# Kernel tuning notes

Measured on AMD Instinct MI355X. Metric: run time of the kernel, lower is better.

Reference implementation:

```python
import jax, jax.numpy as jnp
import numpy as np

D = 768
H = 12
HD = D // H
EPS = 1e-8  # torch cosine_similarity default eps


def setup_inputs() -> dict:
    key = jax.random.key(0)
    ks = jax.random.split(key, 16)
    bs, T, K = 8, 2048, 512
    s = 0.02
    return {
        "hidden_states": jax.random.normal(ks[0], (bs, T, D), jnp.float32),
        "attention_mask": jnp.ones((bs, T), jnp.int32),
        "pooled_hidden_states": jax.random.normal(ks[1], (bs, D), jnp.float32),
        "kg_key": jax.random.normal(ks[2], (bs, K, D), jnp.float32),
        "kg_value": jax.random.normal(ks[3], (bs, K, D), jnp.float32),
        "beta": jnp.ones((H,), jnp.float32),
        "Wq": jax.random.normal(ks[4], (D, D), jnp.float32) * s,
        "bq": jnp.zeros((D,), jnp.float32),
        "Wk": jax.random.normal(ks[5], (D, D), jnp.float32) * s,
        "bk": jnp.zeros((D,), jnp.float32),
        "Wv": jax.random.normal(ks[6], (D, D), jnp.float32) * s,
        "bv": jnp.zeros((D,), jnp.float32),
        "Wo": jax.random.normal(ks[7], (D, D), jnp.float32) * s,
        "bo": jnp.zeros((D,), jnp.float32),
    }


def reference(hidden_states, attention_mask, pooled_hidden_states, kg_key, kg_value,
              beta, Wq, bq, Wk, bk, Wv, bv, Wo, bo):
    bs, T, _ = hidden_states.shape
    K = kg_key.shape[1]
    # cosine similarity between pooled state and each KG key: [bs, K]
    pn = pooled_hidden_states / jnp.maximum(
        jnp.linalg.norm(pooled_hidden_states, axis=-1, keepdims=True), EPS)
    kn = kg_key / jnp.maximum(jnp.linalg.norm(kg_key, axis=-1, keepdims=True), EPS)
    sim = jnp.einsum("bd,bkd->bk", pn, kn)

    scale = HD ** -0.5
    # projections (torch Linear: y = x @ W.T + b)
    q = ((hidden_states @ Wq.T + bq) * scale).reshape(bs, T, H, HD).transpose(0, 2, 1, 3)
    k = (kg_value @ Wk.T + bk).reshape(bs, K, H, HD).transpose(0, 2, 1, 3)
    v = (kg_value @ Wv.T + bv).reshape(bs, K, H, HD).transpose(0, 2, 1, 3)

    # scores + per-head cosine-sim bias: [bs, H, T, K]
    scores = jnp.einsum("bhtd,bhkd->bhtk", q, k)
    scores = scores + beta[None, :, None, None] * sim[:, None, None, :]
    probs = jax.nn.softmax(scores, axis=-1)

    out = jnp.einsum("bhtk,bhkd->bhtd", probs, v)
    out = out.transpose(0, 2, 1, 3).reshape(bs, T, D)
    return out @ Wo.T + bo
```

## Files before the change

kernel.cpp:

```cpp
#include <hip/hip_runtime.h>
#include <math.h>

#define D_MODEL 768
#define NHEAD   12
#define HD      64
#define SEQ_T   2048
#define SEQ_K   512
#define BS      8
#define EPS_COS 1e-8f
#define LOG2E   1.44269504f

typedef short  bf16x8 __attribute__((ext_vector_type(8)));
typedef float  f32x4  __attribute__((ext_vector_type(4)));

__device__ __forceinline__ ushort f2bf(float x) {
    unsigned b = __float_as_uint(x);
    return (ushort)((b + 0x7FFF + ((b >> 16) & 1)) >> 16);
}
__device__ __forceinline__ unsigned cvt_pk_bf16(float lo, float hi) {
    unsigned r;
    asm("v_cvt_pk_bf16_f32 %0, %1, %2" : "=v"(r) : "v"(lo), "v"(hi));
    return r;
}
__device__ __forceinline__ float exp2_fast(float x) {
    float r;
    asm("v_exp_f32 %0, %1" : "=v"(r) : "v"(x));
    return r;
}

__device__ __forceinline__ void async_copy16(void* lds_base, const void* g_src) {
    __builtin_amdgcn_global_load_lds(
        (const __attribute__((address_space(1))) unsigned int*)g_src,
        (__attribute__((address_space(3))) unsigned int*)lds_base,
        16, 0, 0);
}

__global__ __launch_bounds__(256) void cvt4_kernel(
    const float* __restrict__ s0, const float* __restrict__ s1,
    const float* __restrict__ s2, const float* __restrict__ s3,
    ushort* __restrict__ d0, ushort* __restrict__ d1,
    ushort* __restrict__ d2, ushort* __restrict__ d3)
{
    const float* s; ushort* d;
    switch (blockIdx.y) {
        case 0: s = s0; d = d0; break;
        case 1: s = s1; d = d1; break;
        case 2: s = s2; d = d2; break;
        default: s = s3; d = d3; break;
    }
    int i = blockIdx.x * 256 + threadIdx.x;
    float4 v = reinterpret_cast<const float4*>(s)[i];
    ushort4 o;
    o.x = f2bf(v.x); o.y = f2bf(v.y); o.z = f2bf(v.z); o.w = f2bf(v.w);
    reinterpret_cast<ushort4*>(d)[i] = o;
}

__global__ __launch_bounds__(256) void sim_kernel(
    const float* __restrict__ pooled, const float* __restrict__ kg_key,
    const float* __restrict__ beta, float* __restrict__ bsim)
{
    int wid  = (blockIdx.x * blockDim.x + threadIdx.x) >> 6;
    int lane = threadIdx.x & 63;
    int b  = wid >> 9;
    int kk = wid & 511;
    const float* p   = pooled + (size_t)b * D_MODEL;
    const float* key = kg_key + ((size_t)b * SEQ_K + kk) * D_MODEL;
    float dpk = 0.f, dkk = 0.f, dpp = 0.f;
    for (int i = lane; i < D_MODEL; i += 64) {
        float pv = p[i], kv = key[i];
        dpk += pv * kv; dkk += kv * kv; dpp += pv * pv;
    }
    for (int off = 32; off; off >>= 1) {
        dpk += __shfl_xor(dpk, off);
        dkk += __shfl_xor(dkk, off);
        dpp += __shfl_xor(dpp, off);
    }
    if (lane == 0) {
        float np_ = fmaxf(sqrtf(dpp), EPS_COS);
        float nk_ = fmaxf(sqrtf(dkk), EPS_COS);
        float sv = (dpk / (np_ * nk_)) * LOG2E;
#pragma unroll
        for (int h = 0; h < NHEAD; ++h)
            bsim[(size_t)(b * NHEAD + h) * SEQ_K + kk] = beta[h] * sv;
    }
}

__global__ __launch_bounds__(256, 3) void gemm_q_a32_kernel(
    const float* __restrict__ A, const ushort* __restrict__ W,
    const float* __restrict__ bias, ushort* __restrict__ out_bf, float scale)
{
    constexpr int Kd = D_MODEL;
    __shared__ __align__(16) float  AsF[128 * 64];
    __shared__ __align__(16) ushort Bs[128 * 64];
    const int tid = threadIdx.x, wid = tid >> 6, l = tid & 63;
    const int g = l >> 4, c = l & 15;
    const int m0 = blockIdx.x * 128, n0 = blockIdx.y * 128;
    const int wm = (wid >> 1) * 64, wn = (wid & 1) * 64;

    f32x4 acc[4][4] = {};

    for (int k0 = 0; k0 < Kd; k0 += 64) {
        __syncthreads();
#pragma unroll
        for (int it = 0; it < 8; ++it) {
            int L = wid * 8192 + it * 1024 + l * 16;
            int row = L >> 8;
            int blk = (L >> 4) & 15;
            int gb = (blk & 8) | ((blk & 7) ^ (row & 7));
            async_copy16((char*)AsF + wid * 8192 + it * 1024,
                         A + (size_t)(m0 + row) * Kd + k0 + gb * 4);
        }
#pragma unroll
        for (int it = 0; it < 4; ++it) {
            int L = wid * 4096 + it * 1024 + l * 16;
            int row = L >> 7;
            int gb = ((L >> 4) & 7) ^ (row & 7);
            async_copy16((char*)Bs + wid * 4096 + it * 1024,
                         W + (size_t)(n0 + row) * Kd + k0 + gb * 8);
        }
        __syncthreads();

        bf16x8 af[4][2], bf[4][2];
#pragma unroll
        for (int mt = 0; mt < 4; ++mt)
#pragma unroll
            for (int ks = 0; ks < 2; ++ks) {
                int row = wm + mt * 16 + c;
                int b0 = ks * 8 + 2 * g;
                int p0 = (b0 & 8) | ((b0 & 7) ^ (row & 7));
                int p1 = (b0 & 8) | (((b0 + 1) & 7) ^ (row & 7));
                f32x4 a0 = *(const f32x4*)((const char*)AsF + row * 256 + (p0 << 4));
                f32x4 a1 = *(const f32x4*)((const char*)AsF + row * 256 + (p1 << 4));
                union { unsigned u[4]; bf16x8 v; } t;
                t.u[0] = cvt_pk_bf16(a0[0], a0[1]);
                t.u[1] = cvt_pk_bf16(a0[2], a0[3]);
                t.u[2] = cvt_pk_bf16(a1[0], a1[1]);
                t.u[3] = cvt_pk_bf16(a1[2], a1[3]);
                af[mt][ks] = t.v;
            }
#pragma unroll
        for (int nt = 0; nt < 4; ++nt)
#pragma unroll
            for (int ks = 0; ks < 2; ++ks) {
                int row = wn + nt * 16 + c;
                bf[nt][ks] = *(const bf16x8*)((const char*)Bs + row * 128 +
                                              (((ks * 4 + g) ^ (row & 7)) << 4));
            }
        __builtin_amdgcn_s_setprio(1);
#pragma unroll
        for (int mt = 0; mt < 4; ++mt)
#pragma unroll
            for (int nt = 0; nt < 4; ++nt) {
                acc[mt][nt] = __builtin_amdgcn_mfma_f32_16x16x32_bf16(
                    af[mt][0], bf[nt][0], acc[mt][nt], 0, 0, 0);
                acc[mt][nt] = __builtin_amdgcn_mfma_f32_16x16x32_bf16(
                    af[mt][1], bf[nt][1], acc[mt][nt], 0, 0, 0);
            }
        __builtin_amdgcn_s_setprio(0);
    }

#pragma unroll
    for (int mt = 0; mt < 4; ++mt)
#pragma unroll
        for (int nt = 0; nt < 4; ++nt) {
            int col = n0 + wn + nt * 16 + c;
            float bv = bias[col];
#pragma unroll
            for (int j = 0; j < 4; ++j) {
                int row = m0 + wm + mt * 16 + g * 4 + j;
                out_bf[(size_t)row * Kd + col] = f2bf((acc[mt][nt][j] + bv) * scale);
            }
        }
}

__global__ __launch_bounds__(256, 3) void gemm_kv_a32_kernel(
    const float* __restrict__ A,
    const ushort* __restrict__ Wk_, const float* __restrict__ bk_,
    const ushort* __restrict__ Wv_, const float* __restrict__ bv_,
    ushort* __restrict__ outk, ushort* __restrict__ vt)
{
    constexpr int Kd = D_MODEL;
    __shared__ __align__(16) float  AsF[64 * 64];
    __shared__ __align__(16) ushort Bk[64 * 64];
    __shared__ __align__(16) ushort Bv[64 * 64];
    const int tid = threadIdx.x, wid = tid >> 6, l = tid & 63;
    const int g = l >> 4, c = l & 15;
    const int m0 = blockIdx.x * 64, h = blockIdx.y, n0 = h * 64;
    const int wm = (wid >> 1) * 32, wn = (wid & 1) * 32;

    f32x4 acck[2][2] = {}, accv[2][2] = {};

    for (int k0 = 0; k0 < Kd; k0 += 64) {
        __syncthreads();
#pragma unroll
        for (int it = 0; it < 4; ++it) {
            int L = wid * 4096 + it * 1024 + l * 16;
            int row = L >> 8;
            int blk = (L >> 4) & 15;
            int gb = (blk & 8) | ((blk & 7) ^ (row & 7));
            async_copy16((char*)AsF + wid * 4096 + it * 1024,
                         A + (size_t)(m0 + row) * Kd + k0 + gb * 4);
        }
#pragma unroll
        for (int it = 0; it < 2; ++it) {
            int L = wid * 2048 + it * 1024 + l * 16;
            int row = L >> 7;
            int gb = ((L >> 4) & 7) ^ (row & 7);
            async_copy16((char*)Bk + wid * 2048 + it * 1024,
                         Wk_ + (size_t)(n0 + row) * Kd + k0 + gb * 8);
            async_copy16((char*)Bv + wid * 2048 + it * 1024,
                         Wv_ + (size_t)(n0 + row) * Kd + k0 + gb * 8);
        }
        __syncthreads();

        bf16x8 af[2][2], bkf[2][2], bvf[2][2];
#pragma unroll
        for (int mt = 0; mt < 2; ++mt)
#pragma unroll
            for (int ks = 0; ks < 2; ++ks) {
                int row = wm + mt * 16 + c;
                int b0 = ks * 8 + 2 * g;
                int p0 = (b0 & 8) | ((b0 & 7) ^ (row & 7));
                int p1 = (b0 & 8) | (((b0 + 1) & 7) ^ (row & 7));
                f32x4 a0 = *(const f32x4*)((const char*)AsF + row * 256 + (p0 << 4));
                f32x4 a1 = *(const f32x4*)((const char*)AsF + row * 256 + (p1 << 4));
                union { unsigned u[4]; bf16x8 v; } t;
                t.u[0] = cvt_pk_bf16(a0[0], a0[1]);
                t.u[1] = cvt_pk_bf16(a0[2], a0[3]);
                t.u[2] = cvt_pk_bf16(a1[0], a1[1]);
                t.u[3] = cvt_pk_bf16(a1[2], a1[3]);
                af[mt][ks] = t.v;
            }
#pragma unroll
        for (int nt = 0; nt < 2; ++nt)
#pragma unroll
            for (int ks = 0; ks < 2; ++ks) {
                int row = wn + nt * 16 + c;
                int off = row * 128 + (((ks * 4 + g) ^ (row & 7)) << 4);
                bkf[nt][ks] = *(const bf16x8*)((const char*)Bk + off);
                bvf[nt][ks] = *(const bf16x8*)((const char*)Bv + off);
            }
        __builtin_amdgcn_s_setprio(1);
#pragma unroll
        for (int mt = 0; mt < 2; ++mt)
#pragma unroll
            for (int nt = 0; nt < 2; ++nt)
#pragma unroll
                for (int ks = 0; ks < 2; ++ks) {
                    acck[mt][nt] = __builtin_amdgcn_mfma_f32_16x16x32_bf16(
                        af[mt][ks], bkf[nt][ks], acck[mt][nt], 0, 0, 0);
                    accv[mt][nt] = __builtin_amdgcn_mfma_f32_16x16x32_bf16(
                        af[mt][ks], bvf[nt][ks], accv[mt][nt], 0, 0, 0);
                }
        __builtin_amdgcn_s_setprio(0);
    }

#pragma unroll
    for (int mt = 0; mt < 2; ++mt)
#pragma unroll
        for (int nt = 0; nt < 2; ++nt) {
            int col = n0 + wn + nt * 16 + c;
            float bbk = bk_[col];
#pragma unroll
            for (int j = 0; j < 4; ++j) {
                int row = m0 + wm + mt * 16 + 4 * g + j;
                outk[(size_t)row * Kd + col] = f2bf(acck[mt][nt][j] + bbk);
            }
        }

    {
        int b = m0 >> 9;
        int kc = (m0 >> 7) & 3;
#pragma unroll
        for (int mt = 0; mt < 2; ++mt) {
            int kb0 = (m0 & 64) + wm + mt * 16 + 4 * g;
            int kp0 = ((kb0 >> 5) << 5) | (((kb0 >> 2) & 3) << 3) | (((kb0 >> 4) & 1) << 2);
#pragma unroll
            for (int nt = 0; nt < 2; ++nt) {
                int d = wn + nt * 16 + c;
                float bbv = bv_[n0 + d];
                unsigned u0 = cvt_pk_bf16(accv[mt][nt][0] + bbv, accv[mt][nt][1] + bbv);
                unsigned u1 = cvt_pk_bf16(accv[mt][nt][2] + bbv, accv[mt][nt][3] + bbv);
                size_t base = ((size_t)(b * NHEAD + h) * HD + d) * SEQ_K + kc * 128 + kp0;
                uint2 st2; st2.x = u0; st2.y = u1;
                *(uint2*)(vt + base) = st2;
            }
        }
    }
}

__global__ __launch_bounds__(256, 2) void gemm_o_kernel(
    const ushort* __restrict__ A, const ushort* __restrict__ W,
    const float* __restrict__ bias, float* __restrict__ out_f32)
{
    constexpr int Kd = D_MODEL;
    __shared__ __align__(16) ushort As[128 * 64];
    __shared__ __align__(16) ushort Bs[128 * 64];
    const int tid = threadIdx.x, wid = tid >> 6, l = tid & 63;
    const int g = l >> 4, c = l & 15;
    const int m0 = blockIdx.x * 128, n0 = blockIdx.y * 128;
    const int wm = (wid >> 1) * 64, wn = (wid & 1) * 64;

    f32x4 acc[4][4] = {};

    for (int k0 = 0; k0 < Kd; k0 += 64) {
        __syncthreads();
#pragma unroll
        for (int it = 0; it < 4; ++it) {
            int L = wid * 4096 + it * 1024 + l * 16;
            int row = L >> 7;
            int gb = ((L >> 4) & 7) ^ (row & 7);
            async_copy16((char*)As + wid * 4096 + it * 1024,
                         A + (size_t)(m0 + row) * Kd + k0 + gb * 8);
        }
#pragma unroll
        for (int it = 0; it < 4; ++it) {
            int L = wid * 4096 + it * 1024 + l * 16;
            int row = L >> 7;
            int gb = ((L >> 4) & 7) ^ (row & 7);
            async_copy16((char*)Bs + wid * 4096 + it * 1024,
                         W + (size_t)(n0 + row) * Kd + k0 + gb * 8);
        }
        __syncthreads();

        bf16x8 af[4][2], bf[4][2];
#pragma unroll
        for (int mt = 0; mt < 4; ++mt)
#pragma unroll
            for (int ks = 0; ks < 2; ++ks) {
                int row = wm + mt * 16 + c;
                af[mt][ks] = *(const bf16x8*)((const char*)As + row * 128 +
                                              (((ks * 4 + g) ^ (row & 7)) << 4));
            }
#pragma unroll
        for (int nt = 0; nt < 4; ++nt)
#pragma unroll
            for (int ks = 0; ks < 2; ++ks) {
                int row = wn + nt * 16 + c;
                bf[nt][ks] = *(const bf16x8*)((const char*)Bs + row * 128 +
                                              (((ks * 4 + g) ^ (row & 7)) << 4));
            }
        __builtin_amdgcn_s_setprio(1);
#pragma unroll
        for (int mt = 0; mt < 4; ++mt)
#pragma unroll
            for (int nt = 0; nt < 4; ++nt) {
                acc[mt][nt] = __builtin_amdgcn_mfma_f32_16x16x32_bf16(
                    af[mt][0], bf[nt][0], acc[mt][nt], 0, 0, 0);
                acc[mt][nt] = __builtin_amdgcn_mfma_f32_16x16x32_bf16(
                    af[mt][1], bf[nt][1], acc[mt][nt], 0, 0, 0);
            }
        __builtin_amdgcn_s_setprio(0);
    }

#pragma unroll
    for (int mt = 0; mt < 4; ++mt)
#pragma unroll
        for (int nt = 0; nt < 4; ++nt) {
            int col = n0 + wn + nt * 16 + c;
            float bv = bias[col];
#pragma unroll
            for (int j = 0; j < 4; ++j) {
                int row = m0 + wm + mt * 16 + g * 4 + j;
                out_f32[(size_t)row * Kd + col] = acc[mt][nt][j] + bv;
            }
        }
}

__global__ __launch_bounds__(256, 4) void attn_mfma_kernel(
    const ushort* __restrict__ qb, const ushort* __restrict__ kbp,
    const ushort* __restrict__ vt, const float* __restrict__ bsim,
    ushort* __restrict__ ctx)
{
    int bid = blockIdx.x;
    int w = (bid & 7) * 384 + (bid >> 3);
    int tt = w & 31; int rest = w >> 5; int h = rest % 12; int b = rest / 12;
    int t0 = tt * 64;
    int tid = threadIdx.x, wid = tid >> 6, l = tid & 63;
    int g = l >> 4, c = l & 15;

    __shared__ __align__(16) ushort Ks[128 * 64];
    __shared__ __align__(16) ushort Vs[64 * 128];

    const ushort* srck[4]; const ushort* srcv[4];
    char* dstk[4]; char* dstv[4];
#pragma unroll
    for (int it = 0; it < 4; ++it) {
        int L = wid * 4096 + it * 1024 + l * 16;
        int row = L >> 7;
        int gb = ((L >> 4) & 7) ^ (row & 7);
        srck[it] = kbp + (size_t)(b * SEQ_K + row) * D_MODEL + h * HD + gb * 8;
        dstk[it] = (char*)Ks + wid * 4096 + it * 1024;
        int d = L >> 8;
        int blk = (L >> 4) & 15;
        int gblk = (blk & 8) | ((blk & 7) ^ (d & 7));
        srcv[it] = vt + ((size_t)((b * NHEAD + h) * HD + d)) * SEQ_K + gblk * 8;
        dstv[it] = (char*)Vs + wid * 4096 + it * 1024;
    }

#pragma unroll
    for (int it = 0; it < 2; ++it) {
        int L = wid * 2048 + it * 1024 + l * 16;
        int row = L >> 7;
        int gb = ((L >> 4) & 7) ^ (row & 7);
        async_copy16((char*)Vs + wid * 2048 + it * 1024,
                     qb + (size_t)(b * SEQ_T + t0 + row) * D_MODEL + h * HD + gb * 8);
    }
#pragma unroll
    for (int it = 0; it < 4; ++it) async_copy16(dstk[it], srck[it]);
    const float* bsrow = bsim + (size_t)(b * NHEAD + h) * SEQ_K;
    __syncthreads();

    bf16x8 aq[2];
#pragma unroll
    for (int ks = 0; ks < 2; ++ks) {
        int row = wid * 16 + c;
        aq[ks] = *(const bf16x8*)((const char*)Vs + row * 128 +
                                  (((ks * 4 + g) ^ (row & 7)) << 4));
    }
    __syncthreads();

    const bf16x8 ones8 = {(short)0x3F80, (short)0x3F80, (short)0x3F80, (short)0x3F80,
                          (short)0x3F80, (short)0x3F80, (short)0x3F80, (short)0x3F80};
    f32x4 oacc[4] = {};
    f32x4 oSum = {};

    for (int kc = 0; kc < 4; ++kc) {
#pragma unroll
        for (int it = 0; it < 4; ++it) {
            async_copy16(dstv[it], srcv[it]);
            srcv[it] += 128;
        }
        f32x4 st[8];
        __builtin_amdgcn_s_setprio(1);
#pragma unroll
        for (int nt = 0; nt < 8; ++nt) {
            f32x4 cinit = *(const f32x4*)(bsrow + kc * 128 + nt * 16 + 4 * g);
            int krow = nt * 16 + c;
            bf16x8 ak0 = *(const bf16x8*)((const char*)Ks + krow * 128 +
                                          ((g ^ (krow & 7)) << 4));
            st[nt] = __builtin_amdgcn_mfma_f32_16x16x32_bf16(
                ak0, aq[0], cinit, 0, 0, 0);
            bf16x8 ak1 = *(const bf16x8*)((const char*)Ks + krow * 128 +
                                          (((4 + g) ^ (krow & 7)) << 4));
            st[nt] = __builtin_amdgcn_mfma_f32_16x16x32_bf16(
                ak1, aq[1], st[nt], 0, 0, 0);
        }
        __builtin_amdgcn_s_setprio(0);

#pragma unroll
        for (int nt = 0; nt < 8; ++nt)
#pragma unroll
            for (int j = 0; j < 4; ++j) st[nt][j] = exp2_fast(st[nt][j]);

        __syncthreads();

        if (kc < 3) {
#pragma unroll
            for (int it = 0; it < 4; ++it) {
                srck[it] += 128 * D_MODEL;
                async_copy16(dstk[it], srck[it]);
            }
        }

        bf16x8 pa[4];
#pragma unroll
        for (int kb = 0; kb < 4; ++kb) {
            union { unsigned u[4]; bf16x8 v; } pk;
            pk.u[0] = cvt_pk_bf16(st[2 * kb][0],     st[2 * kb][1]);
            pk.u[1] = cvt_pk_bf16(st[2 * kb][2],     st[2 * kb][3]);
            pk.u[2] = cvt_pk_bf16(st[2 * kb + 1][0], st[2 * kb + 1][1]);
            pk.u[3] = cvt_pk_bf16(st[2 * kb + 1][2], st[2 * kb + 1][3]);
            pa[kb] = pk.v;
        }
        __builtin_amdgcn_s_setprio(1);
#pragma unroll
        for (int kb = 0; kb < 4; ++kb) {
            oSum = __builtin_amdgcn_mfma_f32_16x16x32_bf16(
                pa[kb], ones8, oSum, 0, 0, 0);
#pragma unroll
            for (int dt = 0; dt < 4; ++dt) {
                int d = dt * 16 + c;
                int blk = kb * 4 + g;
                int sb = (blk & 8) | ((blk & 7) ^ (d & 7));
                bf16x8 bv = *(const bf16x8*)((const char*)Vs + d * 256 + sb * 16);
                oacc[dt] = __builtin_amdgcn_mfma_f32_16x16x32_bf16(
                    pa[kb], bv, oacc[dt], 0, 0, 0);
            }
        }
        __builtin_amdgcn_s_setprio(0);
        __syncthreads();
    }

    f32x4 invL;
#pragma unroll
    for (int j = 0; j < 4; ++j) invL[j] = 1.f / oSum[j];
#pragma unroll
    for (int dt = 0; dt < 4; ++dt)
#pragma unroll
        for (int j = 0; j < 4; ++j) {
            int trow = t0 + wid * 16 + 4 * g + j;
            int d = dt * 16 + c;
            ctx[(size_t)(b * SEQ_T + trow) * D_MODEL + h * HD + d] =
                f2bf(oacc[dt][j] * invL[j]);
        }
}

extern "C" void kernel_launch(void* const* d_in, const int* in_sizes, int n_in,
                              void* d_out, int out_size, void* d_ws, size_t ws_size,
                              hipStream_t stream)
{
    const float* hidden  = (const float*)d_in[0];
    const float* pooled  = (const float*)d_in[2];
    const float* kg_key  = (const float*)d_in[3];
    const float* kg_val  = (const float*)d_in[4];
    const float* beta    = (const float*)d_in[5];
    const float* Wq = (const float*)d_in[6];  const float* bq = (const float*)d_in[7];
    const float* Wk = (const float*)d_in[8];  const float* bk = (const float*)d_in[9];
    const float* Wv = (const float*)d_in[10]; const float* bv = (const float*)d_in[11];
    const float* Wo = (const float*)d_in[12]; const float* bo = (const float*)d_in[13];
    float* out = (float*)d_out;

    const size_t MQ = (size_t)BS * SEQ_T;
    const size_t MK = (size_t)BS * SEQ_K;
    const size_t DW = D_MODEL * D_MODEL;

    float*  bsim = (float*)d_ws;
    ushort* wqb  = (ushort*)(bsim + BS * NHEAD * SEQ_K);
    ushort* wkb  = wqb + DW;
    ushort* wvb  = wkb + DW;
    ushort* wob  = wvb + DW;
    ushort* qbb  = wob + DW;
    ushort* kbb  = qbb + MQ * D_MODEL;
    ushort* vtb  = kbb + MK * D_MODEL;
    ushort* ctxb = vtb + MK * D_MODEL;

    cvt4_kernel<<<dim3(DW / 4 / 256, 4), 256, 0, stream>>>(
        Wq, Wk, Wv, Wo, wqb, wkb, wvb, wob);

    sim_kernel<<<(BS * SEQ_K) / 4, 256, 0, stream>>>(pooled, kg_key, beta, bsim);

    gemm_q_a32_kernel<<<dim3(MQ / 128, 6), 256, 0, stream>>>(
        hidden, wqb, bq, qbb, 0.125f * LOG2E);
    gemm_kv_a32_kernel<<<dim3(MK / 64, 12), 256, 0, stream>>>(
        kg_val, wkb, bk, wvb, bv, kbb, vtb);

    attn_mfma_kernel<<<BS * NHEAD * (SEQ_T / 64), 256, 0, stream>>>(
        qbb, kbb, vtb, bsim, ctxb);

    gemm_o_kernel<<<dim3(MQ / 128, 6), 256, 0, stream>>>(ctxb, wob, bo, out);
}
```

Before: 128.3 us.

## Read Q, K, V fragments directly from global memory instead of LDS staging

```diff
diff --git a/kernel.cpp b/kernel.cpp
--- a/kernel.cpp
+++ b/kernel.cpp
@@ -379,70 +379,32 @@
     int tid = threadIdx.x, wid = tid >> 6, l = tid & 63;
     int g = l >> 4, c = l & 15;
 
-    __shared__ __align__(16) ushort Ks[128 * 64];
-    __shared__ __align__(16) ushort Vs[64 * 128];
-
-    const ushort* srck[4]; const ushort* srcv[4];
-    char* dstk[4]; char* dstv[4];
-#pragma unroll
-    for (int it = 0; it < 4; ++it) {
-        int L = wid * 4096 + it * 1024 + l * 16;
-        int row = L >> 7;
-        int gb = ((L >> 4) & 7) ^ (row & 7);
-        srck[it] = kbp + (size_t)(b * SEQ_K + row) * D_MODEL + h * HD + gb * 8;
-        dstk[it] = (char*)Ks + wid * 4096 + it * 1024;
-        int d = L >> 8;
-        int blk = (L >> 4) & 15;
-        int gblk = (blk & 8) | ((blk & 7) ^ (d & 7));
-        srcv[it] = vt + ((size_t)((b * NHEAD + h) * HD + d)) * SEQ_K + gblk * 8;
-        dstv[it] = (char*)Vs + wid * 4096 + it * 1024;
-    }
-
-#pragma unroll
-    for (int it = 0; it < 2; ++it) {
-        int L = wid * 2048 + it * 1024 + l * 16;
-        int row = L >> 7;
-        int gb = ((L >> 4) & 7) ^ (row & 7);
-        async_copy16((char*)Vs + wid * 2048 + it * 1024,
-                     qb + (size_t)(b * SEQ_T + t0 + row) * D_MODEL + h * HD + gb * 8);
-    }
-#pragma unroll
-    for (int it = 0; it < 4; ++it) async_copy16(dstk[it], srck[it]);
-    const float* bsrow = bsim + (size_t)(b * NHEAD + h) * SEQ_K;
-    __syncthreads();
-
+    const float*  bsrow = bsim + (size_t)(b * NHEAD + h) * SEQ_K;
+    const ushort* qrow = qb + (size_t)(b * SEQ_T + t0 + wid * 16 + c) * D_MODEL + h * HD;
     bf16x8 aq[2];
-#pragma unroll
-    for (int ks = 0; ks < 2; ++ks) {
-        int row = wid * 16 + c;
-        aq[ks] = *(const bf16x8*)((const char*)Vs + row * 128 +
-                                  (((ks * 4 + g) ^ (row & 7)) << 4));
-    }
-    __syncthreads();
+    aq[0] = *(const bf16x8*)(qrow + g * 8);
+    aq[1] = *(const bf16x8*)(qrow + (4 + g) * 8);
+
+    const ushort* krow = kbp + (size_t)(b * SEQ_K + c) * D_MODEL + h * HD;
+    const ushort* vrow = vt + ((size_t)((b * NHEAD + h) * HD) + c) * SEQ_K;
 
     const bf16x8 ones8 = {(short)0x3F80, (short)0x3F80, (short)0x3F80, (short)0x3F80,
                           (short)0x3F80, (short)0x3F80, (short)0x3F80, (short)0x3F80};
     f32x4 oacc[4] = {};
     f32x4 oSum = {};
 
+#pragma unroll
     for (int kc = 0; kc < 4; ++kc) {
-#pragma unroll
-        for (int it = 0; it < 4; ++it) {
-            async_copy16(dstv[it], srcv[it]);
-            srcv[it] += 128;
-        }
         f32x4 st[8];
         __builtin_amdgcn_s_setprio(1);
 #pragma unroll
         for (int nt = 0; nt < 8; ++nt) {
             f32x4 cinit = *(const f32x4*)(bsrow + kc * 128 + nt * 16 + 4 * g);
-            int krow = nt * 16 + c;
-            bf16x8 ak0 = *(const bf16x8*)((const char*)Ks + krow * 128 +
-                                          ((g ^ (krow & 7)) << 4));
+            const ushort* kr = krow + (size_t)(kc * 128 + nt * 16) * D_MODEL;
+            bf16x8 ak0 = *(const bf16x8*)(kr + g * 8);
+            bf16x8 ak1 = *(const bf16x8*)(kr + (4 + g) * 8);
             st[nt] = __builtin_amdgcn_mfma_f32_16x16x32_bf16(
                 ak0, aq[0], cinit, 0, 0, 0);
-            bf16x8 ak1 = *(const bf16x8*)((const char*)Ks + krow * 128 +
-                                          (((4 + g) ^ (krow & 7)) << 4));
             st[nt] = __builtin_amdgcn_mfma_f32_16x16x32_bf16(
                 ak1, aq[1], st[nt], 0, 0, 0);
         }
@@ -452,16 +414,6 @@
         for (int nt = 0; nt < 8; ++nt)
 #pragma unroll
             for (int j = 0; j < 4; ++j) st[nt][j] = exp2_fast(st[nt][j]);
-
-        __syncthreads();
-
-        if (kc < 3) {
-#pragma unroll
-            for (int it = 0; it < 4; ++it) {
-                srck[it] += 128 * D_MODEL;
-                async_copy16(dstk[it], srck[it]);
-            }
-        }
 
         bf16x8 pa[4];
 #pragma unroll
@@ -480,16 +432,13 @@
                 pa[kb], ones8, oSum, 0, 0, 0);
 #pragma unroll
             for (int dt = 0; dt < 4; ++dt) {
-                int d = dt * 16 + c;
-                int blk = kb * 4 + g;
-                int sb = (blk & 8) | ((blk & 7) ^ (d & 7));
-                bf16x8 bv = *(const bf16x8*)((const char*)Vs + d * 256 + sb * 16);
+                bf16x8 bv = *(const bf16x8*)(vrow + (size_t)(dt * 16) * SEQ_K +
+                                             kc * 128 + (kb * 4 + g) * 8);
                 oacc[dt] = __builtin_amdgcn_mfma_f32_16x16x32_bf16(
                     pa[kb], bv, oacc[dt], 0, 0, 0);
             }
         }
         __builtin_amdgcn_s_setprio(0);
-        __syncthreads();
     }
 
     f32x4 invL;
```

Result: slower. 268.0 us (+108.9%).

## Process 128 query rows per attention block to reuse K/V tiles

Applied to the files above, without the earlier changes.

```diff
diff --git a/kernel.cpp b/kernel.cpp
--- a/kernel.cpp
+++ b/kernel.cpp
@@ -367,15 +367,15 @@
         }
 }
 
-__global__ __launch_bounds__(256, 4) void attn_mfma_kernel(
+__global__ __launch_bounds__(256, 2) void attn_mfma_kernel(
     const ushort* __restrict__ qb, const ushort* __restrict__ kbp,
     const ushort* __restrict__ vt, const float* __restrict__ bsim,
     ushort* __restrict__ ctx)
 {
     int bid = blockIdx.x;
-    int w = (bid & 7) * 384 + (bid >> 3);
-    int tt = w & 31; int rest = w >> 5; int h = rest % 12; int b = rest / 12;
-    int t0 = tt * 64;
+    int w = (bid & 7) * 192 + (bid >> 3);
+    int tile = w & 15; int rest = w >> 4; int h = rest % 12; int b = rest / 12;
+    int t0 = tile * 128;
     int tid = threadIdx.x, wid = tid >> 6, l = tid & 63;
     int g = l >> 4, c = l & 15;
 
@@ -399,11 +399,11 @@
     }
 
 #pragma unroll
-    for (int it = 0; it < 2; ++it) {
-        int L = wid * 2048 + it * 1024 + l * 16;
+    for (int it = 0; it < 4; ++it) {
+        int L = wid * 4096 + it * 1024 + l * 16;
         int row = L >> 7;
         int gb = ((L >> 4) & 7) ^ (row & 7);
-        async_copy16((char*)Vs + wid * 2048 + it * 1024,
+        async_copy16((char*)Vs + wid * 4096 + it * 1024,
                      qb + (size_t)(b * SEQ_T + t0 + row) * D_MODEL + h * HD + gb * 8);
     }
 #pragma unroll
@@ -411,19 +411,21 @@
     const float* bsrow = bsim + (size_t)(b * NHEAD + h) * SEQ_K;
     __syncthreads();
 
-    bf16x8 aq[2];
-#pragma unroll
-    for (int ks = 0; ks < 2; ++ks) {
-        int row = wid * 16 + c;
-        aq[ks] = *(const bf16x8*)((const char*)Vs + row * 128 +
-                                  (((ks * 4 + g) ^ (row & 7)) << 4));
-    }
+    bf16x8 aq[2][2];
+#pragma unroll
+    for (int sub = 0; sub < 2; ++sub)
+#pragma unroll
+        for (int ks = 0; ks < 2; ++ks) {
+            int row = wid * 32 + sub * 16 + c;
+            aq[sub][ks] = *(const bf16x8*)((const char*)Vs + row * 128 +
+                                           (((ks * 4 + g) ^ (row & 7)) << 4));
+        }
     __syncthreads();
 
     const bf16x8 ones8 = {(short)0x3F80, (short)0x3F80, (short)0x3F80, (short)0x3F80,
                           (short)0x3F80, (short)0x3F80, (short)0x3F80, (short)0x3F80};
-    f32x4 oacc[4] = {};
-    f32x4 oSum = {};
+    f32x4 oacc0[4] = {}, oacc1[4] = {};
+    f32x4 oSum0 = {}, oSum1 = {};
 
     for (int kc = 0; kc < 4; ++kc) {
 #pragma unroll
@@ -431,7 +433,7 @@
             async_copy16(dstv[it], srcv[it]);
             srcv[it] += 128;
         }
-        f32x4 st[8];
+        f32x4 st0[8], st1[8];
         __builtin_amdgcn_s_setprio(1);
 #pragma unroll
         for (int nt = 0; nt < 8; ++nt) {
@@ -439,19 +441,26 @@
             int krow = nt * 16 + c;
             bf16x8 ak0 = *(const bf16x8*)((const char*)Ks + krow * 128 +
                                           ((g ^ (krow & 7)) << 4));
-            st[nt] = __builtin_amdgcn_mfma_f32_16x16x32_bf16(
-                ak0, aq[0], cinit, 0, 0, 0);
+            st0[nt] = __builtin_amdgcn_mfma_f32_16x16x32_bf16(
+                ak0, aq[0][0], cinit, 0, 0, 0);
+            st1[nt] = __builtin_amdgcn_mfma_f32_16x16x32_bf16(
+                ak0, aq[1][0], cinit, 0, 0, 0);
             bf16x8 ak1 = *(const bf16x8*)((const char*)Ks + krow * 128 +
                                           (((4 + g) ^ (krow & 7)) << 4));
-            st[nt] = __builtin_amdgcn_mfma_f32_16x16x32_bf16(
-                ak1, aq[1], st[nt], 0, 0, 0);
+            st0[nt] = __builtin_amdgcn_mfma_f32_16x16x32_bf16(
+                ak1, aq[0][1], st0[nt], 0, 0, 0);
+            st1[nt] = __builtin_amdgcn_mfma_f32_16x16x32_bf16(
+                ak1, aq[1][1], st1[nt], 0, 0, 0);
         }
         __builtin_amdgcn_s_setprio(0);
 
 #pragma unroll
         for (int nt = 0; nt < 8; ++nt)
 #pragma unroll
-            for (int j = 0; j < 4; ++j) st[nt][j] = exp2_fast(st[nt][j]);
+            for (int j = 0; j < 4; ++j) {
+                st0[nt][j] = exp2_fast(st0[nt][j]);
+                st1[nt][j] = exp2_fast(st1[nt][j]);
+            }
 
         __syncthreads();
 
@@ -463,46 +472,61 @@
             }
         }
 
-        bf16x8 pa[4];
+        bf16x8 pa0[4], pa1[4];
 #pragma unroll
         for (int kb = 0; kb < 4; ++kb) {
             union { unsigned u[4]; bf16x8 v; } pk;
-            pk.u[0] = cvt_pk_bf16(st[2 * kb][0],     st[2 * kb][1]);
-            pk.u[1] = cvt_pk_bf16(st[2 * kb][2],     st[2 * kb][3]);
-            pk.u[2] = cvt_pk_bf16(st[2 * kb + 1][0], st[2 * kb + 1][1]);
-            pk.u[3] = cvt_pk_bf16(st[2 * kb + 1][2], st[2 * kb + 1][3]);
-            pa[kb] = pk.v;
+            pk.u[0] = cvt_pk_bf16(st0[2 * kb][0],     st0[2 * kb][1]);
+            pk.u[1] = cvt_pk_bf16(st0[2 * kb][2],     st0[2 * kb][3]);
+            pk.u[2] = cvt_pk_bf16(st0[2 * kb + 1][0], st0[2 * kb + 1][1]);
+            pk.u[3] = cvt_pk_bf16(st0[2 * kb + 1][2], st0[2 * kb + 1][3]);
+            pa0[kb] = pk.v;
+            pk.u[0] = cvt_pk_bf16(st1[2 * kb][0],     st1[2 * kb][1]);
+            pk.u[1] = cvt_pk_bf16(st1[2 * kb][2],     st1[2 * kb][3]);
+            pk.u[2] = cvt_pk_bf16(st1[2 * kb + 1][0], st1[2 * kb + 1][1]);
+            pk.u[3] = cvt_pk_bf16(st1[2 * kb + 1][2], st1[2 * kb + 1][3]);
+            pa1[kb] = pk.v;
         }
         __builtin_amdgcn_s_setprio(1);
 #pragma unroll
         for (int kb = 0; kb < 4; ++kb) {
-            oSum = __builtin_amdgcn_mfma_f32_16x16x32_bf16(
-                pa[kb], ones8, oSum, 0, 0, 0);
+            oSum0 = __builtin_amdgcn_mfma_f32_16x16x32_bf16(
+                pa0[kb], ones8, oSum0, 0, 0, 0);
+            oSum1 = __builtin_amdgcn_mfma_f32_16x16x32_bf16(
+                pa1[kb], ones8, oSum1, 0, 0, 0);
 #pragma unroll
             for (int dt = 0; dt < 4; ++dt) {
                 int d = dt * 16 + c;
                 int blk = kb * 4 + g;
                 int sb = (blk & 8) | ((blk & 7) ^ (d & 7));
                 bf16x8 bv = *(const bf16x8*)((const char*)Vs + d * 256 + sb * 16);
-                oacc[dt] = __builtin_amdgcn_mfma_f32_16x16x32_bf16(
-                    pa[kb], bv, oacc[dt], 0, 0, 0);
+                oacc0[dt] = __builtin_amdgcn_mfma_f32_16x16x32_bf16(
+                    pa0[kb], bv, oacc0[dt], 0, 0, 0);
+                oacc1[dt] = __builtin_amdgcn_mfma_f32_16x16x32_bf16(
+                    pa1[kb], bv, oacc1[dt], 0, 0, 0);
             }
         }
         __builtin_amdgcn_s_setprio(0);
         __syncthreads();
     }
 
-    f32x4 invL;
-#pragma unroll
-    for (int j = 0; j < 4; ++j) invL[j] = 1.f / oSum[j];
+    f32x4 invL0, invL1;
+#pragma unroll
+    for (int j = 0; j < 4; ++j) {
+        invL0[j] = 1.f / oSum0[j];
+        invL1[j] = 1.f / oSum1[j];
+    }
 #pragma unroll
     for (int dt = 0; dt < 4; ++dt)
 #pragma unroll
         for (int j = 0; j < 4; ++j) {
-            int trow = t0 + wid * 16 + 4 * g + j;
             int d = dt * 16 + c;
-            ctx[(size_t)(b * SEQ_T + trow) * D_MODEL + h * HD + d] =
-                f2bf(oacc[dt][j] * invL[j]);
+            int trow0 = t0 + wid * 32 + 4 * g + j;
+            ctx[(size_t)(b * SEQ_T + trow0) * D_MODEL + h * HD + d] =
+                f2bf(oacc0[dt][j] * invL0[j]);
+            int trow1 = trow0 + 16;
+            ctx[(size_t)(b * SEQ_T + trow1) * D_MODEL + h * HD + d] =
+                f2bf(oacc1[dt][j] * invL1[j]);
         }
 }
 
@@ -545,7 +569,7 @@
     gemm_kv_a32_kernel<<<dim3(MK / 64, 12), 256, 0, stream>>>(
         kg_val, wkb, bk, wvb, bv, kbb, vtb);
 
-    attn_mfma_kernel<<<BS * NHEAD * (SEQ_T / 64), 256, 0, stream>>>(
+    attn_mfma_kernel<<<BS * NHEAD * (SEQ_T / 128), 256, 0, stream>>>(
         qbb, kbb, vtb, bsim, ctxb);
 
     gemm_o_kernel<<<dim3(MQ / 128, 6), 256, 0, stream>>>(ctxb, wob, bo, out);
```

After: 122.6 us. 4.4% less time.

## Enlarge attention tile to 256 query rows with double-buffered K/V

Applied to the files above, without the earlier changes.

```diff
diff --git a/kernel.cpp b/kernel.cpp
--- a/kernel.cpp
+++ b/kernel.cpp
@@ -367,143 +367,161 @@
         }
 }
 
-__global__ __launch_bounds__(256, 4) void attn_mfma_kernel(
+__global__ __launch_bounds__(256, 2) void attn_mfma_kernel(
     const ushort* __restrict__ qb, const ushort* __restrict__ kbp,
     const ushort* __restrict__ vt, const float* __restrict__ bsim,
     ushort* __restrict__ ctx)
 {
     int bid = blockIdx.x;
-    int w = (bid & 7) * 384 + (bid >> 3);
-    int tt = w & 31; int rest = w >> 5; int h = rest % 12; int b = rest / 12;
-    int t0 = tt * 64;
+    int w = (bid & 7) * 96 + (bid >> 3);
+    int tile = w & 7; int rest = w >> 3; int h = rest % 12; int b = rest / 12;
+    int t0 = tile * 256;
     int tid = threadIdx.x, wid = tid >> 6, l = tid & 63;
     int g = l >> 4, c = l & 15;
 
-    __shared__ __align__(16) ushort Ks[128 * 64];
-    __shared__ __align__(16) ushort Vs[64 * 128];
+    __shared__ __align__(16) ushort KV[2][128 * 128];
 
     const ushort* srck[4]; const ushort* srcv[4];
-    char* dstk[4]; char* dstv[4];
+    int offk[4], offv[4];
 #pragma unroll
     for (int it = 0; it < 4; ++it) {
         int L = wid * 4096 + it * 1024 + l * 16;
         int row = L >> 7;
         int gb = ((L >> 4) & 7) ^ (row & 7);
         srck[it] = kbp + (size_t)(b * SEQ_K + row) * D_MODEL + h * HD + gb * 8;
-        dstk[it] = (char*)Ks + wid * 4096 + it * 1024;
+        offk[it] = wid * 4096 + it * 1024;
         int d = L >> 8;
         int blk = (L >> 4) & 15;
         int gblk = (blk & 8) | ((blk & 7) ^ (d & 7));
         srcv[it] = vt + ((size_t)((b * NHEAD + h) * HD + d)) * SEQ_K + gblk * 8;
-        dstv[it] = (char*)Vs + wid * 4096 + it * 1024;
-    }
-
-#pragma unroll
-    for (int it = 0; it < 2; ++it) {
-        int L = wid * 2048 + it * 1024 + l * 16;
+        offv[it] = 16384 + wid * 4096 + it * 1024;
+    }
+
+#pragma unroll
+    for (int it = 0; it < 8; ++it) {
+        int L = wid * 8192 + it * 1024 + l * 16;
         int row = L >> 7;
         int gb = ((L >> 4) & 7) ^ (row & 7);
-        async_copy16((char*)Vs + wid * 2048 + it * 1024,
+        async_copy16((char*)KV[0] + wid * 8192 + it * 1024,
                      qb + (size_t)(b * SEQ_T + t0 + row) * D_MODEL + h * HD + gb * 8);
     }
-#pragma unroll
-    for (int it = 0; it < 4; ++it) async_copy16(dstk[it], srck[it]);
     const float* bsrow = bsim + (size_t)(b * NHEAD + h) * SEQ_K;
     __syncthreads();
 
-    bf16x8 aq[2];
-#pragma unroll
-    for (int ks = 0; ks < 2; ++ks) {
-        int row = wid * 16 + c;
-        aq[ks] = *(const bf16x8*)((const char*)Vs + row * 128 +
-                                  (((ks * 4 + g) ^ (row & 7)) << 4));
-    }
+    bf16x8 aq[4][2];
+#pragma unroll
+    for (int sub = 0; sub < 4; ++sub)
+#pragma unroll
+        for (int ks = 0; ks < 2; ++ks) {
+            int row = wid * 64 + sub * 16 + c;
+            aq[sub][ks] = *(const bf16x8*)((const char*)KV[0] + row * 128 +
+                                           (((ks * 4 + g) ^ (row & 7)) << 4));
+        }
     __syncthreads();
+
+#pragma unroll
+    for (int it = 0; it < 4; ++it) {
+        async_copy16((char*)KV[0] + offk[it], srck[it]);
+        async_copy16((char*)KV[0] + offv[it], srcv[it]);
+    }
 
     const bf16x8 ones8 = {(short)0x3F80, (short)0x3F80, (short)0x3F80, (short)0x3F80,
                           (short)0x3F80, (short)0x3F80, (short)0x3F80, (short)0x3F80};
-    f32x4 oacc[4] = {};
-    f32x4 oSum = {};
+    f32x4 oacc[4][4] = {};
+    f32x4 oSum[4] = {};
+    int cur = 0;
 
     for (int kc = 0; kc < 4; ++kc) {
-#pragma unroll
-        for (int it = 0; it < 4; ++it) {
-            async_copy16(dstv[it], srcv[it]);
-            srcv[it] += 128;
-        }
-        f32x4 st[8];
-        __builtin_amdgcn_s_setprio(1);
-#pragma unroll
-        for (int nt = 0; nt < 8; ++nt) {
-            f32x4 cinit = *(const f32x4*)(bsrow + kc * 128 + nt * 16 + 4 * g);
-            int krow = nt * 16 + c;
-            bf16x8 ak0 = *(const bf16x8*)((const char*)Ks + krow * 128 +
-                                          ((g ^ (krow & 7)) << 4));
-            st[nt] = __builtin_amdgcn_mfma_f32_16x16x32_bf16(
-                ak0, aq[0], cinit, 0, 0, 0);
-            bf16x8 ak1 = *(const bf16x8*)((const char*)Ks + krow * 128 +
-                                          (((4 + g) ^ (krow & 7)) << 4));
-            st[nt] = __builtin_amdgcn_mfma_f32_16x16x32_bf16(
-                ak1, aq[1], st[nt], 0, 0, 0);
-        }
-        __builtin_amdgcn_s_setprio(0);
-
-#pragma unroll
-        for (int nt = 0; nt < 8; ++nt)
-#pragma unroll
-            for (int j = 0; j < 4; ++j) st[nt][j] = exp2_fast(st[nt][j]);
-
-        __syncthreads();
-
+        __syncthreads();
         if (kc < 3) {
+            int nxt = cur ^ 1;
 #pragma unroll
             for (int it = 0; it < 4; ++it) {
                 srck[it] += 128 * D_MODEL;
-                async_copy16(dstk[it], srck[it]);
-            }
-        }
-
-        bf16x8 pa[4];
+                async_copy16((char*)KV[nxt] + offk[it], srck[it]);
+                srcv[it] += 128;
+                async_copy16((char*)KV[nxt] + offv[it], srcv[it]);
+            }
+        }
+        const char* Kb = (const char*)KV[cur];
+        const char* Vb = (const char*)KV[cur] + 16384;
+
 #pragma unroll
         for (int kb = 0; kb < 4; ++kb) {
-            union { unsigned u[4]; bf16x8 v; } pk;
-            pk.u[0] = cvt_pk_bf16(st[2 * kb][0],     st[2 * kb][1]);
-            pk.u[1] = cvt_pk_bf16(st[2 * kb][2],     st[2 * kb][3]);
-            pk.u[2] = cvt_pk_bf16(st[2 * kb + 1][0], st[2 * kb + 1][1]);
-            pk.u[3] = cvt_pk_bf16(st[2 * kb + 1][2], st[2 * kb + 1][3]);
-            pa[kb] = pk.v;
-        }
-        __builtin_amdgcn_s_setprio(1);
-#pragma unroll
-        for (int kb = 0; kb < 4; ++kb) {
-            oSum = __builtin_amdgcn_mfma_f32_16x16x32_bf16(
-                pa[kb], ones8, oSum, 0, 0, 0);
+            f32x4 st[4][2];
+            __builtin_amdgcn_s_setprio(1);
+#pragma unroll
+            for (int n2 = 0; n2 < 2; ++n2) {
+                int nt = 2 * kb + n2;
+                f32x4 cinit = *(const f32x4*)(bsrow + kc * 128 + nt * 16 + 4 * g);
+                int krow = nt * 16 + c;
+                bf16x8 ak0 = *(const bf16x8*)(Kb + krow * 128 +
+                                              ((g ^ (krow & 7)) << 4));
+                bf16x8 ak1 = *(const bf16x8*)(Kb + krow * 128 +
+                                              (((4 + g) ^ (krow & 7)) << 4));
+#pragma unroll
+                for (int sub = 0; sub < 4; ++sub) {
+                    st[sub][n2] = __builtin_amdgcn_mfma_f32_16x16x32_bf16(
+                        ak0, aq[sub][0], cinit, 0, 0, 0);
+                    st[sub][n2] = __builtin_amdgcn_mfma_f32_16x16x32_bf16(
+                        ak1, aq[sub][1], st[sub][n2], 0, 0, 0);
+                }
+            }
+            __builtin_amdgcn_s_setprio(0);
+
+            bf16x8 pa[4];
+#pragma unroll
+            for (int sub = 0; sub < 4; ++sub) {
+                f32x4 e0, e1;
+#pragma unroll
+                for (int j = 0; j < 4; ++j) {
+                    e0[j] = exp2_fast(st[sub][0][j]);
+                    e1[j] = exp2_fast(st[sub][1][j]);
+                }
+                union { unsigned u[4]; bf16x8 v; } pk;
+                pk.u[0] = cvt_pk_bf16(e0[0], e0[1]);
+                pk.u[1] = cvt_pk_bf16(e0[2], e0[3]);
+                pk.u[2] = cvt_pk_bf16(e1[0], e1[1]);
+                pk.u[3] = cvt_pk_bf16(e1[2], e1[3]);
+                pa[sub] = pk.v;
+            }
+
+            __builtin_amdgcn_s_setprio(1);
+#pragma unroll
+            for (int sub = 0; sub < 4; ++sub)
+                oSum[sub] = __builtin_amdgcn_mfma_f32_16x16x32_bf16(
+                    pa[sub], ones8, oSum[sub], 0, 0, 0);
 #pragma unroll
             for (int dt = 0; dt < 4; ++dt) {
                 int d = dt * 16 + c;
                 int blk = kb * 4 + g;
                 int sb = (blk & 8) | ((blk & 7) ^ (d & 7));
-                bf16x8 bv = *(const bf16x8*)((const char*)Vs + d * 256 + sb * 16);
-                oacc[dt] = __builtin_amdgcn_mfma_f32_16x16x32_bf16(
-                    pa[kb], bv, oacc[dt], 0, 0, 0);
-            }
-        }
-        __builtin_amdgcn_s_setprio(0);
-        __syncthreads();
-    }
-
-    f32x4 invL;
-#pragma unroll
-    for (int j = 0; j < 4; ++j) invL[j] = 1.f / oSum[j];
-#pragma unroll
-    for (int dt = 0; dt < 4; ++dt)
-#pragma unroll
-        for (int j = 0; j < 4; ++j) {
-            int trow = t0 + wid * 16 + 4 * g + j;
-            int d = dt * 16 + c;
-            ctx[(size_t)(b * SEQ_T + trow) * D_MODEL + h * HD + d] =
-                f2bf(oacc[dt][j] * invL[j]);
-        }
+                bf16x8 bv = *(const bf16x8*)(Vb + d * 256 + sb * 16);
+#pragma unroll
+                for (int sub = 0; sub < 4; ++sub)
+                    oacc[sub][dt] = __builtin_amdgcn_mfma_f32_16x16x32_bf16(
+                        pa[sub], bv, oacc[sub][dt], 0, 0, 0);
+            }
+            __builtin_amdgcn_s_setprio(0);
+        }
+        cur ^= 1;
+    }
+
+#pragma unroll
+    for (int sub = 0; sub < 4; ++sub) {
+        f32x4 invL;
+#pragma unroll
+        for (int j = 0; j < 4; ++j) invL[j] = 1.f / oSum[sub][j];
+#pragma unroll
+        for (int dt = 0; dt < 4; ++dt)
+#pragma unroll
+            for (int j = 0; j < 4; ++j) {
+                int trow = t0 + wid * 64 + sub * 16 + 4 * g + j;
+                int d = dt * 16 + c;
+                ctx[(size_t)(b * SEQ_T + trow) * D_MODEL + h * HD + d] =
+                    f2bf(oacc[sub][dt][j] * invL[j]);
+            }
+    }
 }
 
 extern "C" void kernel_launch(void* const* d_in, const int* in_sizes, int n_in,
@@ -545,7 +563,7 @@
     gemm_kv_a32_kernel<<<dim3(MK / 64, 12), 256, 0, stream>>>(
         kg_val, wkb, bk, wvb, bv, kbb, vtb);
 
-    attn_mfma_kernel<<<BS * NHEAD * (SEQ_T / 64), 256, 0, stream>>>(
+    attn_mfma_kernel<<<BS * NHEAD * (SEQ_T / 256), 256, 0, stream>>>(
         qbb, kbb, vtb, bsim, ctxb);
 
     gemm_o_kernel<<<dim3(MQ / 128, 6), 256, 0, stream>>>(ctxb, wob, bo, out);
```

After: 126.0 us. No clear change (-1.8%).
